# Performance work log

Hardware: AMD Instinct MI355X
Metric: run time of the kernel (lower is better)

The kernel has to match this reference:

```python
import jax, jax.numpy as jnp
import numpy as np

WS = 8  # window size
NH = 4  # heads
EPS = 1e-5

def _rel_pos_index(ws):
    coords = np.stack(np.meshgrid(np.arange(ws), np.arange(ws), indexing='ij')).reshape(2, -1)
    rel = coords[:, :, None] - coords[:, None, :]
    rel[0] += ws - 1
    rel[1] += ws - 1
    rel[0] *= 2 * ws - 1
    return jnp.asarray(rel.sum(0))  # (ws*ws, ws*ws) int

REL_IDX = _rel_pos_index(WS)

def group_norm1(x, g, b):
    # GroupNorm(1, C): normalize over (C,H,W) per sample, per-channel affine
    m = jnp.mean(x, axis=(1, 2, 3), keepdims=True)
    v = jnp.var(x, axis=(1, 2, 3), keepdims=True)
    return (x - m) * jax.lax.rsqrt(v + EPS) * g[None, :, None, None] + b[None, :, None, None]

def conv1x1(x, w, b):
    return jnp.einsum('oc,bchw->bohw', w, x) + b[None, :, None, None]

def win_attn(x, qkv_w, qkv_b, out_w, out_b, bias_tab):
    # x: (B,H,W,C); non-shifted Swin window attention with gathered rel-pos bias
    B, H, W, C = x.shape
    hd = C // NH
    L = WS * WS
    scale = hd ** -0.5
    nh_, nw_ = H // WS, W // WS
    xw = x.reshape(B, nh_, WS, nw_, WS, C).transpose(0, 1, 3, 2, 4, 5).reshape(-1, L, C)
    qkv = (xw @ qkv_w.T + qkv_b).reshape(-1, L, 3, NH, hd)
    q = jnp.transpose(qkv[:, :, 0], (0, 2, 1, 3))  # (N,NH,L,hd)
    k = jnp.transpose(qkv[:, :, 1], (0, 2, 1, 3))
    v = jnp.transpose(qkv[:, :, 2], (0, 2, 1, 3))
    bias = bias_tab[:, REL_IDX.reshape(-1)].reshape(NH, L, L)
    attn = jax.nn.softmax(jnp.einsum('nhqd,nhkd->nhqk', q, k) * scale + bias[None], axis=-1)
    o = jnp.einsum('nhqk,nhkd->nhqd', attn, v).transpose(0, 2, 1, 3).reshape(-1, L, C)
    o = o @ out_w.T + out_b
    return o.reshape(B, nh_, nw_, WS, WS, C).transpose(0, 1, 3, 2, 4, 5).reshape(B, H, W, C)

def ffn(x, g, b, w1, b1, w2, b2):
    h = group_norm1(x, g, b)
    h = jax.nn.gelu(conv1x1(h, w1, b1), approximate=False)
    return conv1x1(h, w2, b2)

def setup_inputs() -> dict:
    key = jax.random.key(0)
    B, D, H, W = 8, 192, 128, 128
    ks = jax.random.split(key, 16)
    s = 0.02
    return {
        'sem': jax.random.normal(ks[0], (B, D, H, W), jnp.float32),
        'depth_feat': jax.random.normal(ks[1], (B, D, H, W), jnp.float32),
        'ns_g': jnp.ones((D,), jnp.float32), 'ns_b': jnp.zeros((D,), jnp.float32),
        'nd_g': jnp.ones((D,), jnp.float32), 'nd_b': jnp.zeros((D,), jnp.float32),
        'wd2s': jax.random.normal(ks[2], (D, D), jnp.float32) * s, 'bd2s': jnp.zeros((D,), jnp.float32),
        'ws2d': jax.random.normal(ks[3], (D, D), jnp.float32) * s, 'bs2d': jnp.zeros((D,), jnp.float32),
        'alpha': jnp.float32(0.1), 'beta': jnp.float32(0.1),
        'qkv_sem_w': jax.random.normal(ks[4], (3 * D, D), jnp.float32) * s, 'qkv_sem_b': jnp.zeros((3 * D,), jnp.float32),
        'out_sem_w': jax.random.normal(ks[5], (D, D), jnp.float32) * s, 'out_sem_b': jnp.zeros((D,), jnp.float32),
        'qkv_dep_w': jax.random.normal(ks[6], (3 * D, D), jnp.float32) * s, 'qkv_dep_b': jnp.zeros((3 * D,), jnp.float32),
        'out_dep_w': jax.random.normal(ks[7], (D, D), jnp.float32) * s, 'out_dep_b': jnp.zeros((D,), jnp.float32),
        'rel_pos_bias': jax.random.normal(ks[8], (NH, (2 * WS - 1) ** 2), jnp.float32) * s,
        'fs_g': jnp.ones((D,), jnp.float32), 'fs_b': jnp.zeros((D,), jnp.float32),
        'fs_w1': jax.random.normal(ks[9], (2 * D, D), jnp.float32) * s, 'fs_b1': jnp.zeros((2 * D,), jnp.float32),
        'fs_w2': jax.random.normal(ks[10], (D, 2 * D), jnp.float32) * s, 'fs_b2': jnp.zeros((D,), jnp.float32),
        'fd_g': jnp.ones((D,), jnp.float32), 'fd_b': jnp.zeros((D,), jnp.float32),
        'fd_w1': jax.random.normal(ks[11], (2 * D, D), jnp.float32) * s, 'fd_b1': jnp.zeros((2 * D,), jnp.float32),
        'fd_w2': jax.random.normal(ks[12], (D, 2 * D), jnp.float32) * s, 'fd_b2': jnp.zeros((D,), jnp.float32),
    }

def reference(sem, depth_feat, ns_g, ns_b, nd_g, nd_b, wd2s, bd2s, ws2d, bs2d, alpha, beta,
              qkv_sem_w, qkv_sem_b, out_sem_w, out_sem_b, qkv_dep_w, qkv_dep_b, out_dep_w, out_dep_b,
              rel_pos_bias, fs_g, fs_b, fs_w1, fs_b1, fs_w2, fs_b2, fd_g, fd_b, fd_w1, fd_b1, fd_w2, fd_b2):
    sem_n = group_norm1(sem, ns_g, ns_b)
    depth_n = group_norm1(depth_feat, nd_g, nd_b)
    sem_in = sem_n + alpha * jax.nn.sigmoid(conv1x1(depth_n, wd2s, bd2s))
    dep_in = depth_n + beta * jax.nn.sigmoid(conv1x1(sem_n, ws2d, bs2d))
    sem_hw = jnp.transpose(sem_in, (0, 2, 3, 1))  # (B,H,W,C)
    dep_hw = jnp.transpose(dep_in, (0, 2, 3, 1))
    sem_a = win_attn(sem_hw, qkv_sem_w, qkv_sem_b, out_sem_w, out_sem_b, rel_pos_bias)
    dep_a = win_attn(dep_hw, qkv_dep_w, qkv_dep_b, out_dep_w, out_dep_b, rel_pos_bias)
    sem_out = sem + jnp.transpose(sem_a, (0, 3, 1, 2))
    dep_out = depth_feat + jnp.transpose(dep_a, (0, 3, 1, 2))
    sem_out = sem_out + ffn(sem_out, fs_g, fs_b, fs_w1, fs_b1, fs_w2, fs_b2)
    dep_out = dep_out + ffn(dep_out, fd_g, fd_b, fd_w1, fd_b1, fd_w2, fd_b2)
    return (sem_out, dep_out)
```

## Files before the change

kernel.cpp:

```cpp
#include <hip/hip_runtime.h>

typedef unsigned short u16;
typedef float f32x4 __attribute__((ext_vector_type(4)));
typedef int   i32x4 __attribute__((ext_vector_type(4)));
typedef short bf16x8 __attribute__((ext_vector_type(8)));

#define CCH    192
#define HW     16384
#define NPIX   131072
#define NELEM  25165824
#define NSAMP  3145728

__device__ __forceinline__ float b2f(u16 u) {
  return __uint_as_float(((unsigned)u) << 16);
}
__device__ __forceinline__ u16 f2b(float f) {
  unsigned u = __float_as_uint(f);
  unsigned r = (u + 0x7fffu + ((u >> 16) & 1u)) >> 16;
  return (u16)r;
}
__device__ __forceinline__ void unpack8(i32x4 v, float* f) {
#pragma unroll
  for (int i = 0; i < 4; i++) {
    unsigned u = (unsigned)v[i];
    f[2 * i]     = __uint_as_float(u << 16);
    f[2 * i + 1] = __uint_as_float(u & 0xffff0000u);
  }
}
__device__ __forceinline__ i32x4 pack8(const float* f) {
  i32x4 r;
#pragma unroll
  for (int i = 0; i < 4; i++) {
    unsigned lo = f2b(f[2 * i]);
    unsigned hi = f2b(f[2 * i + 1]);
    r[i] = (int)(lo | (hi << 16));
  }
  return r;
}

__global__ __launch_bounds__(256) void stats_partial(
    const float* __restrict__ A, const float* __restrict__ B,
    float* __restrict__ acc, int slotbase) {
  const float* src = (blockIdx.z == 0) ? A : B;
  int sample = blockIdx.y;
  size_t base = (size_t)sample * NSAMP + (size_t)blockIdx.x * 32768;
  float s = 0.f, q = 0.f;
  for (int it = 0; it < 16; it++) {
    const float* ptr = src + base + it * 2048 + threadIdx.x * 8;
    f32x4 v0 = *(const f32x4*)ptr;
    f32x4 v1 = *(const f32x4*)(ptr + 4);
#pragma unroll
    for (int i = 0; i < 4; i++) {
      s += v0[i] + v1[i];
      q += v0[i] * v0[i] + v1[i] * v1[i];
    }
  }
#pragma unroll
  for (int o = 32; o > 0; o >>= 1) {
    s += __shfl_down(s, o);
    q += __shfl_down(q, o);
  }
  __shared__ float red[8];
  int wv = threadIdx.x >> 6;
  if ((threadIdx.x & 63) == 0) { red[wv * 2] = s; red[wv * 2 + 1] = q; }
  __syncthreads();
  if (threadIdx.x == 0) {
    float S = red[0] + red[2] + red[4] + red[6];
    float Q = red[1] + red[3] + red[5] + red[7];
    int e = ((slotbase + blockIdx.z) * 8 + sample) * 2;
    atomicAdd(&acc[e], S);
    atomicAdd(&acc[e + 1], Q);
  }
}

__global__ void finalize_stats(const float* __restrict__ acc,
                               float* __restrict__ mr, int entbase, int nent) {
  int i = threadIdx.x;
  if (i < nent) {
    int e = entbase + i;
    float s = acc[e * 2], q = acc[e * 2 + 1];
    const float invN = 1.0f / (float)NSAMP;
    float mean = s * invN;
    float var = q * invN - mean * mean;
    mr[e * 2] = mean;
    mr[e * 2 + 1] = rsqrtf(var + 1e-5f);
  }
}

__global__ __launch_bounds__(256) void norm_t(
    const float* __restrict__ in, u16* __restrict__ outp,
    const float* __restrict__ g, const float* __restrict__ bb,
    const float* __restrict__ mr, int slot) {
  __shared__ u16 tile[128 * 201];
  int yy = blockIdx.x, b = blockIdx.y;
  int e = (slot * 8 + b) * 2;
  float mean = mr[e], rstd = mr[e + 1];
  int tid = threadIdx.x;
  for (int task = tid; task < 3072; task += 256) {
    int c = task >> 4, xc = task & 15;
    const float* p = in + (size_t)(b * CCH + c) * HW + yy * 128 + xc * 8;
    f32x4 v0 = *(const f32x4*)p;
    f32x4 v1 = *(const f32x4*)(p + 4);
    float sc = rstd * g[c];
    float of = bb[c] - mean * sc;
#pragma unroll
    for (int i = 0; i < 4; i++) {
      tile[(xc * 8 + i) * 201 + c]       = f2b(v0[i] * sc + of);
      tile[(xc * 8 + 4 + i) * 201 + c]   = f2b(v1[i] * sc + of);
    }
  }
  __syncthreads();
  size_t ob = ((size_t)b * HW + (size_t)yy * 128) * CCH;
  for (int task = tid; task < 3072; task += 256) {
    int xx = task / 24, cc = task % 24;
    i32x4 v;
#pragma unroll
    for (int i = 0; i < 4; i++) {
      unsigned lo = tile[xx * 201 + cc * 8 + 2 * i];
      unsigned hi = tile[xx * 201 + cc * 8 + 2 * i + 1];
      v[i] = (int)(lo | (hi << 16));
    }
    *(i32x4*)(outp + ob + (size_t)xx * CCH + cc * 8) = v;
  }
}

__global__ void build_bias(const float* __restrict__ relb,
                           float* __restrict__ biasx) {
  int tid = threadIdx.x;
  for (int i = tid; i < 16384; i += 256) {
    int r    = i & 3;
    int lane = (i >> 2) & 63;
    int nj   = (i >> 8) & 3;
    int mi   = (i >> 10) & 3;
    int h    = (i >> 12) & 3;
    int q = 16 * mi + (lane >> 4) * 4 + r;
    int k = 16 * nj + (lane & 15);
    int qy = q >> 3, qx = q & 7, ky = k >> 3, kx = k & 7;
    biasx[i] = relb[h * 225 + (qy - ky + 7) * 15 + (qx - kx + 7)];
  }
}

struct WPtrs { const float* p[10]; };

__global__ __launch_bounds__(256) void convw(WPtrs wp, u16* __restrict__ dst) {
  const int sz[10]  = {36864, 36864, 110592, 110592, 36864, 36864,
                       73728, 73728, 73728, 73728};
  const int off[10] = {0, 36864, 73728, 184320, 294912, 331776,
                       368640, 442368, 516096, 589824};
  int m = blockIdx.y;
  int i = (blockIdx.x * 256 + threadIdx.x) * 8;
  if (i >= sz[m]) return;
  const float* s = wp.p[m];
  f32x4 a = *(const f32x4*)(s + i);
  f32x4 b = *(const f32x4*)(s + i + 4);
  float f[8] = {a[0], a[1], a[2], a[3], b[0], b[1], b[2], b[3]};
  *(i32x4*)(dst + off[m] + i) = pack8(f);
}

__global__ __launch_bounds__(256) void attn_kernel(
    const u16* __restrict__ qkv, const float* __restrict__ biasx,
    u16* __restrict__ outp) {
  __shared__ u16 kp[4][64 * 72];
  __shared__ u16 vt[4][48 * 72];
  int tid = threadIdx.x;
  int h = tid >> 6, lane = tid & 63;
  int l15 = lane & 15, g4 = lane >> 4;
  int win = blockIdx.x;
  int b = win >> 8, wy = (win >> 4) & 15, wx = win & 15;
  int pbase = (b << 14) + (wy * 8) * 128 + wx * 8;

  for (int task = tid; task < 1536; task += 256) {
    int tok = task / 24;
    int r24 = task - tok * 24;
    int hh = r24 / 6;
    int c = r24 - hh * 6;
    int p = pbase + (tok >> 3) * 128 + (tok & 7);
    i32x4 v = *(const i32x4*)(qkv + (size_t)p * 576 + 192 + hh * 48 + c * 8);
    *(i32x4*)&kp[hh][tok * 72 + c * 8] = v;
  }
  {
    i32x4 z = {0, 0, 0, 0};
    for (int task = tid; task < 512; task += 256) {
      int hh = task >> 7, rem = task & 127, tok = rem >> 1, c = rem & 1;
      *(i32x4*)&kp[hh][tok * 72 + 48 + c * 8] = z;
    }
  }
  for (int task = tid; task < 1536; task += 256) {
    int chidx = task >> 6, tok = task & 63;
    int hh = chidx / 6, c = chidx - hh * 6;
    int p = pbase + (tok >> 3) * 128 + (tok & 7);
    i32x4 v = *(const i32x4*)(qkv + (size_t)p * 576 + 384 + hh * 48 + c * 8);
#pragma unroll
    for (int i = 0; i < 4; i++) {
      unsigned u = (unsigned)v[i];
      vt[hh][(c * 8 + 2 * i) * 72 + tok]     = (u16)(u & 0xffffu);
      vt[hh][(c * 8 + 2 * i + 1) * 72 + tok] = (u16)(u >> 16);
    }
  }
  __syncthreads();

  int ptok[4];
#pragma unroll
  for (int mi = 0; mi < 4; mi++) {
    int t = 16 * mi + l15;
    ptok[mi] = pbase + (t >> 3) * 128 + (t & 7);
  }
  f32x4 acc[4][4];
#pragma unroll
  for (int i = 0; i < 4; i++)
#pragma unroll
    for (int j = 0; j < 4; j++) {
      f32x4 z = {0.f, 0.f, 0.f, 0.f};
      acc[i][j] = z;
    }
#pragma unroll
  for (int s = 0; s < 2; s++) {
    bf16x8 qf[4], kf[4];
#pragma unroll
    for (int mi = 0; mi < 4; mi++)
      qf[mi] = *(const bf16x8*)(qkv + (size_t)ptok[mi] * 576 + h * 48 + s * 32 + g4 * 8);
#pragma unroll
    for (int nj = 0; nj < 4; nj++)
      kf[nj] = *(const bf16x8*)&kp[h][(16 * nj + l15) * 72 + s * 32 + g4 * 8];
#pragma unroll
    for (int mi = 0; mi < 4; mi++)
#pragma unroll
      for (int nj = 0; nj < 4; nj++)
        acc[mi][nj] = __builtin_amdgcn_mfma_f32_16x16x32_bf16(qf[mi], kf[nj], acc[mi][nj], 0, 0, 0);
  }

  const float scale = 0.14433756729740643f;
  float sums[4][4];
#pragma unroll
  for (int mi = 0; mi < 4; mi++) {
#pragma unroll
    for (int r = 0; r < 4; r++) sums[mi][r] = 0.f;
#pragma unroll
    for (int nj = 0; nj < 4; nj++) {
      f32x4 bv = *(const f32x4*)&biasx[(((h * 4 + mi) * 4 + nj) * 64 + lane) * 4];
#pragma unroll
      for (int r = 0; r < 4; r++) {
        float sv = acc[mi][nj][r] * scale + bv[r];
        sv = fminf(fmaxf(sv, -60.f), 60.f);
        float e = __expf(sv);
        acc[mi][nj][r] = e;
        sums[mi][r] += e;
      }
    }
  }
#pragma unroll
  for (int mi = 0; mi < 4; mi++)
#pragma unroll
    for (int r = 0; r < 4; r++) {
      float s = sums[mi][r];
      s += __shfl_xor(s, 1);
      s += __shfl_xor(s, 2);
      s += __shfl_xor(s, 4);
      s += __shfl_xor(s, 8);
      sums[mi][r] = 1.0f / s;
    }
#pragma unroll
  for (int mi = 0; mi < 4; mi++)
#pragma unroll
    for (int nj = 0; nj < 4; nj++)
#pragma unroll
      for (int r = 0; r < 4; r++)
        kp[h][(16 * mi + g4 * 4 + r) * 72 + 16 * nj + l15] = f2b(acc[mi][nj][r]);

  f32x4 oacc[4][3];
#pragma unroll
  for (int i = 0; i < 4; i++)
#pragma unroll
    for (int j = 0; j < 3; j++) {
      f32x4 z = {0.f, 0.f, 0.f, 0.f};
      oacc[i][j] = z;
    }
#pragma unroll
  for (int s = 0; s < 2; s++) {
    bf16x8 pf[4], vf[3];
#pragma unroll
    for (int mi = 0; mi < 4; mi++)
      pf[mi] = *(const bf16x8*)&kp[h][(16 * mi + l15) * 72 + s * 32 + g4 * 8];
#pragma unroll
    for (int n = 0; n < 3; n++)
      vf[n] = *(const bf16x8*)&vt[h][(16 * n + l15) * 72 + s * 32 + g4 * 8];
#pragma unroll
    for (int mi = 0; mi < 4; mi++)
#pragma unroll
      for (int n = 0; n < 3; n++)
        oacc[mi][n] = __builtin_amdgcn_mfma_f32_16x16x32_bf16(pf[mi], vf[n], oacc[mi][n], 0, 0, 0);
  }

#pragma unroll
  for (int mi = 0; mi < 4; mi++)
#pragma unroll
    for (int n = 0; n < 3; n++)
#pragma unroll
      for (int r = 0; r < 4; r++)
        kp[h][(16 * mi + g4 * 4 + r) * 72 + 16 * n + l15] =
            f2b(oacc[mi][n][r] * sums[mi][r]);
  __syncthreads();
  for (int task = tid; task < 1536; task += 256) {
    int tok = task / 24;
    int r24 = task - tok * 24;
    int hh = r24 / 6;
    int c = r24 - hh * 6;
    int p = pbase + (tok >> 3) * 128 + (tok & 7);
    *(i32x4*)(outp + (size_t)p * 192 + hh * 48 + c * 8) =
        *(const i32x4*)&kp[hh][tok * 72 + c * 8];
  }
}

enum { GM_BIAS = 0, GM_GATE = 1, GM_GELU = 2, GM_RES = 3 };

template <int MODE, int KT>
__global__ __launch_bounds__(256, 3) void gemm3(
    const u16* __restrict__ X, const u16* __restrict__ Wb,
    const float* __restrict__ bias, const void* __restrict__ aux,
    void* __restrict__ outv, const float* __restrict__ scale_ptr,
    float* __restrict__ stats_acc, int statslot, int OB, int O) {
  __shared__ union {
    u16 xs[128 * 200];
    float y[8704];
  } sm;
  int tid = threadIdx.x;
  int lane = tid & 63, wave = tid >> 6;
  int l15 = lane & 15, q8 = lane >> 4;
  int wm = (wave & 1) * 64, wn = (wave >> 1) * 32;

  int nwg = gridDim.x;
  int cpx = nwg >> 3;
  int bid = blockIdx.x;
  int id = (bid & 7) * cpx + (bid >> 3);
  int pt = id / OB;
  int p0 = pt * 128;
  int o0 = (id - pt * OB) * 64;

  f32x4 acc[4][2];
#pragma unroll
  for (int i = 0; i < 4; i++)
#pragma unroll
    for (int j = 0; j < 2; j++) {
      f32x4 z = {0.f, 0.f, 0.f, 0.f};
      acc[i][j] = z;
    }

  const u16* brow0 = Wb + (size_t)(o0 + wn + l15) * KT + q8 * 8;
  const u16* brow1 = Wb + (size_t)(o0 + wn + 16 + l15) * KT + q8 * 8;

#pragma unroll
  for (int c = 0; c < KT / 192; c++) {
#pragma unroll
    for (int i = 0; i < 12; i++) {
      int idx = tid + i * 256;
      int row = idx / 24;
      int col = idx - row * 24;
      i32x4 v = *(const i32x4*)(X + (size_t)(p0 + row) * KT + c * 192 + col * 8);
      *(i32x4*)&sm.xs[row * 200 + col * 8] = v;
    }
    __syncthreads();
#pragma unroll
    for (int kc = 0; kc < 6; kc++) {
      bf16x8 b0 = *(const bf16x8*)(brow0 + c * 192 + kc * 32);
      bf16x8 b1 = *(const bf16x8*)(brow1 + c * 192 + kc * 32);
      bf16x8 a0 = *(const bf16x8*)&sm.xs[(wm + l15) * 200 + kc * 32 + q8 * 8];
      bf16x8 a1 = *(const bf16x8*)&sm.xs[(wm + 16 + l15) * 200 + kc * 32 + q8 * 8];
      bf16x8 a2 = *(const bf16x8*)&sm.xs[(wm + 32 + l15) * 200 + kc * 32 + q8 * 8];
      bf16x8 a3 = *(const bf16x8*)&sm.xs[(wm + 48 + l15) * 200 + kc * 32 + q8 * 8];
      acc[0][0] = __builtin_amdgcn_mfma_f32_16x16x32_bf16(a0, b0, acc[0][0], 0, 0, 0);
      acc[0][1] = __builtin_amdgcn_mfma_f32_16x16x32_bf16(a0, b1, acc[0][1], 0, 0, 0);
      acc[1][0] = __builtin_amdgcn_mfma_f32_16x16x32_bf16(a1, b0, acc[1][0], 0, 0, 0);
      acc[1][1] = __builtin_amdgcn_mfma_f32_16x16x32_bf16(a1, b1, acc[1][1], 0, 0, 0);
      acc[2][0] = __builtin_amdgcn_mfma_f32_16x16x32_bf16(a2, b0, acc[2][0], 0, 0, 0);
      acc[2][1] = __builtin_amdgcn_mfma_f32_16x16x32_bf16(a2, b1, acc[2][1], 0, 0, 0);
      acc[3][0] = __builtin_amdgcn_mfma_f32_16x16x32_bf16(a3, b0, acc[3][0], 0, 0, 0);
      acc[3][1] = __builtin_amdgcn_mfma_f32_16x16x32_bf16(a3, b1, acc[3][1], 0, 0, 0);
    }
    __syncthreads();
  }

#pragma unroll
  for (int mi = 0; mi < 4; mi++)
#pragma unroll
    for (int n = 0; n < 2; n++) {
      int pl = wm + mi * 16 + q8 * 4;
      int ol = wn + n * 16 + l15;
      if (MODE == GM_RES) {
        *(f32x4*)&sm.y[ol * 132 + pl] = acc[mi][n];
      } else {
#pragma unroll
        for (int r = 0; r < 4; r++) sm.y[(pl + r) * 68 + ol] = acc[mi][n][r];
      }
    }
  __syncthreads();

  if (MODE == GM_RES) {
    const float* auxf = (const float*)aux;
    float* outf = (float*)outv;
    int o2 = tid >> 2;
    int pc = (tid & 3) * 32;
    int og = o0 + o2;
    int bi = p0 >> 14;
    int r0 = (p0 + pc) & (HW - 1);
    size_t idx = ((size_t)(bi * CCH + og) << 14) + r0;
    float bv = bias[og];
    float s = 0.f, q = 0.f;
#pragma unroll
    for (int i = 0; i < 8; i++) {
      f32x4 vy = *(const f32x4*)&sm.y[o2 * 132 + pc + i * 4];
      f32x4 av = *(const f32x4*)(auxf + idx + i * 4);
      f32x4 w;
#pragma unroll
      for (int j = 0; j < 4; j++) {
        float t = av[j] + vy[j] + bv;
        w[j] = t; s += t; q += t * t;
      }
      *(f32x4*)(outf + idx + i * 4) = w;
    }
    if (statslot >= 0) {
#pragma unroll
      for (int d = 32; d > 0; d >>= 1) {
        s += __shfl_down(s, d);
        q += __shfl_down(q, d);
      }
      if (lane == 0) {
        int e = (statslot + bi) * 2;
        atomicAdd(&stats_acc[e], s);
        atomicAdd(&stats_acc[e + 1], q);
      }
    }
  } else {
    int pl = tid >> 1;
    int oc = (tid & 1) * 32;
    float vals[32];
#pragma unroll
    for (int i = 0; i < 8; i++) {
      f32x4 v = *(const f32x4*)&sm.y[pl * 68 + oc + i * 4];
      vals[i * 4] = v[0]; vals[i * 4 + 1] = v[1];
      vals[i * 4 + 2] = v[2]; vals[i * 4 + 3] = v[3];
    }
    int og0 = o0 + oc;
    size_t rowb = (size_t)(p0 + pl) * (size_t)O + og0;
    u16* outb = (u16*)outv;
    const u16* auxb = (const u16*)aux;
    float sc = 0.f;
    float afv[32];
    if (MODE == GM_GATE) {
      sc = scale_ptr[0];
#pragma unroll
      for (int i = 0; i < 4; i++) {
        i32x4 av = *(const i32x4*)(auxb + rowb + i * 8);
        unpack8(av, &afv[i * 8]);
      }
    }
    float f[32];
#pragma unroll
    for (int i = 0; i < 32; i++) {
      float v = vals[i] + bias[og0 + i];
      if (MODE == GM_GATE) {
        float sg = 1.0f / (1.0f + __expf(-v));
        v = afv[i] + sc * sg;
      } else if (MODE == GM_GELU) {
        v = 0.5f * v * (1.0f + erff(v * 0.70710678118654752f));
      }
      f[i] = v;
    }
#pragma unroll
    for (int i = 0; i < 4; i++)
      *(i32x4*)(outb + rowb + i * 8) = pack8(&f[i * 8]);
  }
}

extern "C" void kernel_launch(void* const* d_in, const int* in_sizes, int n_in,
                              void* d_out, int out_size, void* d_ws,
                              size_t ws_size, hipStream_t stream) {
  (void)in_sizes; (void)n_in; (void)out_size; (void)ws_size;
  const float* sem       = (const float*)d_in[0];
  const float* dep       = (const float*)d_in[1];
  const float* ns_g      = (const float*)d_in[2];
  const float* ns_b      = (const float*)d_in[3];
  const float* nd_g      = (const float*)d_in[4];
  const float* nd_b      = (const float*)d_in[5];
  const float* wd2s      = (const float*)d_in[6];
  const float* bd2s      = (const float*)d_in[7];
  const float* ws2d      = (const float*)d_in[8];
  const float* bs2d      = (const float*)d_in[9];
  const float* alpha     = (const float*)d_in[10];
  const float* beta      = (const float*)d_in[11];
  const float* qkv_sem_w = (const float*)d_in[12];
  const float* qkv_sem_b = (const float*)d_in[13];
  const float* out_sem_w = (const float*)d_in[14];
  const float* out_sem_b = (const float*)d_in[15];
  const float* qkv_dep_w = (const float*)d_in[16];
  const float* qkv_dep_b = (const float*)d_in[17];
  const float* out_dep_w = (const float*)d_in[18];
  const float* out_dep_b = (const float*)d_in[19];
  const float* relb      = (const float*)d_in[20];
  const float* fs_g      = (const float*)d_in[21];
  const float* fs_b      = (const float*)d_in[22];
  const float* fs_w1     = (const float*)d_in[23];
  const float* fs_b1     = (const float*)d_in[24];
  const float* fs_w2     = (const float*)d_in[25];
  const float* fs_b2     = (const float*)d_in[26];
  const float* fd_g      = (const float*)d_in[27];
  const float* fd_b      = (const float*)d_in[28];
  const float* fd_w1     = (const float*)d_in[29];
  const float* fd_b1     = (const float*)d_in[30];
  const float* fd_w2     = (const float*)d_in[31];
  const float* fd_b2     = (const float*)d_in[32];

  float* stats_acc = (float*)d_ws;
  float* mr        = (float*)((char*)d_ws + 256);
  u16* R1 = (u16*)((char*)d_ws + 1024);
  u16* R2 = R1 + NELEM;
  u16* R3 = R2 + NELEM;
  u16* R4 = R3 + NELEM;
  u16* R5 = R4 + NELEM;
  u16* WB = R5 + (size_t)3 * NELEM;
  float* outS = (float*)d_out;
  float* outD = outS + NELEM;
  float* biasx = (float*)R1;

  const u16* WD2S = WB;
  const u16* WS2D = WB + 36864;
  const u16* QKVS = WB + 73728;
  const u16* QKVD = WB + 184320;
  const u16* OUTS = WB + 294912;
  const u16* OUTD = WB + 331776;
  const u16* FSW1 = WB + 368640;
  const u16* FDW1 = WB + 442368;
  const u16* FSW2 = WB + 516096;
  const u16* FDW2 = WB + 589824;

  hipMemsetAsync(d_ws, 0, 512, stream);
  WPtrs wp;
  wp.p[0] = wd2s;      wp.p[1] = ws2d;
  wp.p[2] = qkv_sem_w; wp.p[3] = qkv_dep_w;
  wp.p[4] = out_sem_w; wp.p[5] = out_dep_w;
  wp.p[6] = fs_w1;     wp.p[7] = fd_w1;
  wp.p[8] = fs_w2;     wp.p[9] = fd_w2;
  convw<<<dim3(54, 10), 256, 0, stream>>>(wp, WB);

  stats_partial<<<dim3(96, 8, 2), 256, 0, stream>>>(sem, dep, stats_acc, 0);
  finalize_stats<<<1, 64, 0, stream>>>(stats_acc, mr, 0, 16);
  norm_t<<<dim3(128, 8), 256, 0, stream>>>(sem, R1, ns_g, ns_b, mr, 0);
  norm_t<<<dim3(128, 8), 256, 0, stream>>>(dep, R2, nd_g, nd_b, mr, 1);
  gemm3<GM_GATE, 192><<<3072, 256, 0, stream>>>(R2, WD2S, bd2s, R1, R3, alpha, nullptr, -1, 3, 192);
  gemm3<GM_GATE, 192><<<3072, 256, 0, stream>>>(R1, WS2D, bs2d, R2, R4, beta, nullptr, -1, 3, 192);
  build_bias<<<1, 256, 0, stream>>>(relb, biasx);
  gemm3<GM_BIAS, 192><<<9216, 256, 0, stream>>>(R3, QKVS, qkv_sem_b, nullptr, R5, nullptr, nullptr, -1, 9, 576);
  attn_kernel<<<2048, 256, 0, stream>>>(R5, biasx, R2);
  gemm3<GM_RES, 192><<<3072, 256, 0, stream>>>(R2, OUTS, out_sem_b, sem, outS, nullptr, stats_acc, 16, 3, 192);
  gemm3<GM_BIAS, 192><<<9216, 256, 0, stream>>>(R4, QKVD, qkv_dep_b, nullptr, R5, nullptr, nullptr, -1, 9, 576);
  attn_kernel<<<2048, 256, 0, stream>>>(R5, biasx, R2);
  gemm3<GM_RES, 192><<<3072, 256, 0, stream>>>(R2, OUTD, out_dep_b, dep, outD, nullptr, stats_acc, 24, 3, 192);
  finalize_stats<<<1, 64, 0, stream>>>(stats_acc, mr, 16, 16);
  norm_t<<<dim3(128, 8), 256, 0, stream>>>(outS, R1, fs_g, fs_b, mr, 2);
  norm_t<<<dim3(128, 8), 256, 0, stream>>>(outD, R3, fd_g, fd_b, mr, 3);
  gemm3<GM_GELU, 192><<<6144, 256, 0, stream>>>(R1, FSW1, fs_b1, nullptr, R5, nullptr, nullptr, -1, 6, 384);
  gemm3<GM_RES, 384><<<3072, 256, 0, stream>>>(R5, FSW2, fs_b2, outS, outS, nullptr, nullptr, -1, 3, 192);
  gemm3<GM_GELU, 192><<<6144, 256, 0, stream>>>(R3, FDW1, fd_b1, nullptr, R5, nullptr, nullptr, -1, 6, 384);
  gemm3<GM_RES, 384><<<3072, 256, 0, stream>>>(R5, FDW2, fd_b2, outD, outD, nullptr, nullptr, -1, 3, 192);
}
```

Before: 2.027 ms.

## Shrink GEMM tile to 64x64, use 2D grid, block-reduce stats, polynomial GELU

The pointwise GEMM tile drops from 128 pixels by 64 outputs to 64x64. The grid becomes 2D with no XCD-swizzled block remapping, and the min-occupancy hint is removed. The smaller LDS footprint and fewer accumulators should let more workgroups fit per CU, at the cost of loading each weight tile twice as often and weaker cross-XCD locality. Stats atomics are first reduced inside the block, and exact erff GELU is replaced with the Abramowitz-Stegun polynomial, which changes precision slightly.

```diff
diff --git a/kernel.cpp b/kernel.cpp
--- a/kernel.cpp
+++ b/kernel.cpp
@@ -36,6 +36,19 @@
     r[i] = (int)(lo | (hi << 16));
   }
   return r;
+}
+
+__device__ __forceinline__ float gelu_f(float v) {
+  float ax = fabsf(v) * 0.70710678118654752f;
+  float t = 1.0f / (1.0f + 0.3275911f * ax);
+  float p = t * (0.254829592f +
+           t * (-0.284496736f +
+           t * (1.421413741f +
+           t * (-1.453152027f +
+           t * 1.061405429f))));
+  float er = 1.0f - p * __expf(-ax * ax);
+  er = (v < 0.f) ? -er : er;
+  return 0.5f * v * (1.0f + er);
 }
 
 __global__ __launch_bounds__(256) void stats_partial(
@@ -314,31 +327,26 @@
 enum { GM_BIAS = 0, GM_GATE = 1, GM_GELU = 2, GM_RES = 3 };
 
 template <int MODE, int KT>
-__global__ __launch_bounds__(256, 3) void gemm3(
+__global__ __launch_bounds__(256) void gemm4(
     const u16* __restrict__ X, const u16* __restrict__ Wb,
     const float* __restrict__ bias, const void* __restrict__ aux,
     void* __restrict__ outv, const float* __restrict__ scale_ptr,
-    float* __restrict__ stats_acc, int statslot, int OB, int O) {
+    float* __restrict__ stats_acc, int statslot, int O) {
   __shared__ union {
-    u16 xs[128 * 200];
-    float y[8704];
+    u16 xs[64 * 200];
+    float y[64 * 68];
   } sm;
+  __shared__ float red[8];
   int tid = threadIdx.x;
   int lane = tid & 63, wave = tid >> 6;
   int l15 = lane & 15, q8 = lane >> 4;
-  int wm = (wave & 1) * 64, wn = (wave >> 1) * 32;
-
-  int nwg = gridDim.x;
-  int cpx = nwg >> 3;
-  int bid = blockIdx.x;
-  int id = (bid & 7) * cpx + (bid >> 3);
-  int pt = id / OB;
-  int p0 = pt * 128;
-  int o0 = (id - pt * OB) * 64;
-
-  f32x4 acc[4][2];
-#pragma unroll
-  for (int i = 0; i < 4; i++)
+  int wm = (wave & 1) * 32, wn = (wave >> 1) * 32;
+  int p0 = blockIdx.y * 64;
+  int o0 = blockIdx.x * 64;
+
+  f32x4 acc[2][2];
+#pragma unroll
+  for (int i = 0; i < 2; i++)
 #pragma unroll
     for (int j = 0; j < 2; j++) {
       f32x4 z = {0.f, 0.f, 0.f, 0.f};
@@ -346,17 +354,17 @@
     }
 
   const u16* brow0 = Wb + (size_t)(o0 + wn + l15) * KT + q8 * 8;
-  const u16* brow1 = Wb + (size_t)(o0 + wn + 16 + l15) * KT + q8 * 8;
+  const u16* brow1 = brow0 + (size_t)16 * KT;
 
 #pragma unroll
   for (int c = 0; c < KT / 192; c++) {
 #pragma unroll
-    for (int i = 0; i < 12; i++) {
+    for (int i = 0; i < 6; i++) {
       int idx = tid + i * 256;
       int row = idx / 24;
       int col = idx - row * 24;
-      i32x4 v = *(const i32x4*)(X + (size_t)(p0 + row) * KT + c * 192 + col * 8);
-      *(i32x4*)&sm.xs[row * 200 + col * 8] = v;
+      *(i32x4*)&sm.xs[row * 200 + col * 8] =
+          *(const i32x4*)(X + (size_t)(p0 + row) * KT + c * 192 + col * 8);
     }
     __syncthreads();
 #pragma unroll
@@ -365,28 +373,22 @@
       bf16x8 b1 = *(const bf16x8*)(brow1 + c * 192 + kc * 32);
       bf16x8 a0 = *(const bf16x8*)&sm.xs[(wm + l15) * 200 + kc * 32 + q8 * 8];
       bf16x8 a1 = *(const bf16x8*)&sm.xs[(wm + 16 + l15) * 200 + kc * 32 + q8 * 8];
-      bf16x8 a2 = *(const bf16x8*)&sm.xs[(wm + 32 + l15) * 200 + kc * 32 + q8 * 8];
-      bf16x8 a3 = *(const bf16x8*)&sm.xs[(wm + 48 + l15) * 200 + kc * 32 + q8 * 8];
       acc[0][0] = __builtin_amdgcn_mfma_f32_16x16x32_bf16(a0, b0, acc[0][0], 0, 0, 0);
       acc[0][1] = __builtin_amdgcn_mfma_f32_16x16x32_bf16(a0, b1, acc[0][1], 0, 0, 0);
       acc[1][0] = __builtin_amdgcn_mfma_f32_16x16x32_bf16(a1, b0, acc[1][0], 0, 0, 0);
       acc[1][1] = __builtin_amdgcn_mfma_f32_16x16x32_bf16(a1, b1, acc[1][1], 0, 0, 0);
-      acc[2][0] = __builtin_amdgcn_mfma_f32_16x16x32_bf16(a2, b0, acc[2][0], 0, 0, 0);
-      acc[2][1] = __builtin_amdgcn_mfma_f32_16x16x32_bf16(a2, b1, acc[2][1], 0, 0, 0);
-      acc[3][0] = __builtin_amdgcn_mfma_f32_16x16x32_bf16(a3, b0, acc[3][0], 0, 0, 0);
-      acc[3][1] = __builtin_amdgcn_mfma_f32_16x16x32_bf16(a3, b1, acc[3][1], 0, 0, 0);
     }
     __syncthreads();
   }
 
 #pragma unroll
-  for (int mi = 0; mi < 4; mi++)
+  for (int mi = 0; mi < 2; mi++)
 #pragma unroll
     for (int n = 0; n < 2; n++) {
       int pl = wm + mi * 16 + q8 * 4;
       int ol = wn + n * 16 + l15;
       if (MODE == GM_RES) {
-        *(f32x4*)&sm.y[ol * 132 + pl] = acc[mi][n];
+        *(f32x4*)&sm.y[ol * 68 + pl] = acc[mi][n];
       } else {
 #pragma unroll
         for (int r = 0; r < 4; r++) sm.y[(pl + r) * 68 + ol] = acc[mi][n][r];
@@ -398,7 +400,7 @@
     const float* auxf = (const float*)aux;
     float* outf = (float*)outv;
     int o2 = tid >> 2;
-    int pc = (tid & 3) * 32;
+    int pc = (tid & 3) * 16;
     int og = o0 + o2;
     int bi = p0 >> 14;
     int r0 = (p0 + pc) & (HW - 1);
@@ -406,8 +408,8 @@
     float bv = bias[og];
     float s = 0.f, q = 0.f;
 #pragma unroll
-    for (int i = 0; i < 8; i++) {
-      f32x4 vy = *(const f32x4*)&sm.y[o2 * 132 + pc + i * 4];
+    for (int i = 0; i < 4; i++) {
+      f32x4 vy = *(const f32x4*)&sm.y[o2 * 68 + pc + i * 4];
       f32x4 av = *(const f32x4*)(auxf + idx + i * 4);
       f32x4 w;
 #pragma unroll
@@ -423,18 +425,22 @@
         s += __shfl_down(s, d);
         q += __shfl_down(q, d);
       }
-      if (lane == 0) {
+      if (lane == 0) { red[wave * 2] = s; red[wave * 2 + 1] = q; }
+      __syncthreads();
+      if (tid == 0) {
+        float S = red[0] + red[2] + red[4] + red[6];
+        float Q = red[1] + red[3] + red[5] + red[7];
         int e = (statslot + bi) * 2;
-        atomicAdd(&stats_acc[e], s);
-        atomicAdd(&stats_acc[e + 1], q);
+        atomicAdd(&stats_acc[e], S);
+        atomicAdd(&stats_acc[e + 1], Q);
       }
     }
   } else {
-    int pl = tid >> 1;
-    int oc = (tid & 1) * 32;
-    float vals[32];
-#pragma unroll
-    for (int i = 0; i < 8; i++) {
+    int pl = tid >> 2;
+    int oc = (tid & 3) * 16;
+    float vals[16];
+#pragma unroll
+    for (int i = 0; i < 4; i++) {
       f32x4 v = *(const f32x4*)&sm.y[pl * 68 + oc + i * 4];
       vals[i * 4] = v[0]; vals[i * 4 + 1] = v[1];
       vals[i * 4 + 2] = v[2]; vals[i * 4 + 3] = v[3];
@@ -444,30 +450,29 @@
     u16* outb = (u16*)outv;
     const u16* auxb = (const u16*)aux;
     float sc = 0.f;
-    float afv[32];
+    float afv[16];
     if (MODE == GM_GATE) {
       sc = scale_ptr[0];
 #pragma unroll
-      for (int i = 0; i < 4; i++) {
+      for (int i = 0; i < 2; i++) {
         i32x4 av = *(const i32x4*)(auxb + rowb + i * 8);
         unpack8(av, &afv[i * 8]);
       }
     }
-    float f[32];
-#pragma unroll
-    for (int i = 0; i < 32; i++) {
+    float f[16];
+#pragma unroll
+    for (int i = 0; i < 16; i++) {
       float v = vals[i] + bias[og0 + i];
       if (MODE == GM_GATE) {
         float sg = 1.0f / (1.0f + __expf(-v));
         v = afv[i] + sc * sg;
       } else if (MODE == GM_GELU) {
-        v = 0.5f * v * (1.0f + erff(v * 0.70710678118654752f));
+        v = gelu_f(v);
       }
       f[i] = v;
     }
-#pragma unroll
-    for (int i = 0; i < 4; i++)
-      *(i32x4*)(outb + rowb + i * 8) = pack8(&f[i * 8]);
+    *(i32x4*)(outb + rowb) = pack8(f);
+    *(i32x4*)(outb + rowb + 8) = pack8(f + 8);
   }
 }
 
@@ -545,20 +550,20 @@
   finalize_stats<<<1, 64, 0, stream>>>(stats_acc, mr, 0, 16);
   norm_t<<<dim3(128, 8), 256, 0, stream>>>(sem, R1, ns_g, ns_b, mr, 0);
   norm_t<<<dim3(128, 8), 256, 0, stream>>>(dep, R2, nd_g, nd_b, mr, 1);
-  gemm3<GM_GATE, 192><<<3072, 256, 0, stream>>>(R2, WD2S, bd2s, R1, R3, alpha, nullptr, -1, 3, 192);
-  gemm3<GM_GATE, 192><<<3072, 256, 0, stream>>>(R1, WS2D, bs2d, R2, R4, beta, nullptr, -1, 3, 192);
+  gemm4<GM_GATE, 192><<<dim3(3, 2048), 256, 0, stream>>>(R2, WD2S, bd2s, R1, R3, alpha, nullptr, -1, 192);
+  gemm4<GM_GATE, 192><<<dim3(3, 2048), 256, 0, stream>>>(R1, WS2D, bs2d, R2, R4, beta, nullptr, -1, 192);
   build_bias<<<1, 256, 0, stream>>>(relb, biasx);
-  gemm3<GM_BIAS, 192><<<9216, 256, 0, stream>>>(R3, QKVS, qkv_sem_b, nullptr, R5, nullptr, nullptr, -1, 9, 576);
+  gemm4<GM_BIAS, 192><<<dim3(9, 2048), 256, 0, stream>>>(R3, QKVS, qkv_sem_b, nullptr, R5, nullptr, nullptr, -1, 576);
   attn_kernel<<<2048, 256, 0, stream>>>(R5, biasx, R2);
-  gemm3<GM_RES, 192><<<3072, 256, 0, stream>>>(R2, OUTS, out_sem_b, sem, outS, nullptr, stats_acc, 16, 3, 192);
-  gemm3<GM_BIAS, 192><<<9216, 256, 0, stream>>>(R4, QKVD, qkv_dep_b, nullptr, R5, nullptr, nullptr, -1, 9, 576);
+  gemm4<GM_RES, 192><<<dim3(3, 2048), 256, 0, stream>>>(R2, OUTS, out_sem_b, sem, outS, nullptr, stats_acc, 16, 192);
+  gemm4<GM_BIAS, 192><<<dim3(9, 2048), 256, 0, stream>>>(R4, QKVD, qkv_dep_b, nullptr, R5, nullptr, nullptr, -1, 576);
   attn_kernel<<<2048, 256, 0, stream>>>(R5, biasx, R2);
-  gemm3<GM_RES, 192><<<3072, 256, 0, stream>>>(R2, OUTD, out_dep_b, dep, outD, nullptr, stats_acc, 24, 3, 192);
+  gemm4<GM_RES, 192><<<dim3(3, 2048), 256, 0, stream>>>(R2, OUTD, out_dep_b, dep, outD, nullptr, stats_acc, 24, 192);
   finalize_stats<<<1, 64, 0, stream>>>(stats_acc, mr, 16, 16);
   norm_t<<<dim3(128, 8), 256, 0, stream>>>(outS, R1, fs_g, fs_b, mr, 2);
   norm_t<<<dim3(128, 8), 256, 0, stream>>>(outD, R3, fd_g, fd_b, mr, 3);
-  gemm3<GM_GELU, 192><<<6144, 256, 0, stream>>>(R1, FSW1, fs_b1, nullptr, R5, nullptr, nullptr, -1, 6, 384);
-  gemm3<GM_RES, 384><<<3072, 256, 0, stream>>>(R5, FSW2, fs_b2, outS, outS, nullptr, nullptr, -1, 3, 192);
-  gemm3<GM_GELU, 192><<<6144, 256, 0, stream>>>(R3, FDW1, fd_b1, nullptr, R5, nullptr, nullptr, -1, 6, 384);
-  gemm3<GM_RES, 384><<<3072, 256, 0, stream>>>(R5, FDW2, fd_b2, outD, outD, nullptr, nullptr, -1, 3, 192);
-}
+  gemm4<GM_GELU, 192><<<dim3(6, 2048), 256, 0, stream>>>(R1, FSW1, fs_b1, nullptr, R5, nullptr, nullptr, -1, 384);
+  gemm4<GM_RES, 384><<<dim3(3, 2048), 256, 0, stream>>>(R5, FSW2, fs_b2, outS, outS, nullptr, nullptr, -1, 192);
+  gemm4<GM_GELU, 192><<<dim3(6, 2048), 256, 0, stream>>>(R3, FDW1, fd_b1, nullptr, R5, nullptr, nullptr, -1, 384);
+  gemm4<GM_RES, 384><<<dim3(3, 2048), 256, 0, stream>>>(R5, FDW2, fd_b2, outD, outD, nullptr, nullptr, -1, 192);
+}
```

Result: faster. 1.794 ms (-11.5%).
